# Performance work log

Hardware: AMD Instinct MI355X
Metric: run time of the kernel (lower is better)

## Reference

```python
import jax, jax.numpy as jnp
import numpy as np
import math

DIM = 2048
N_HEADS = 16
N_KV_HEADS = 8
HEAD_DIM = DIM // N_HEADS  # 128
N_REP = N_HEADS // N_KV_HEADS  # 2
BLOCK = 128
TOPK = 8
NEG_INF = -10000.0
SEQ = 4096
BS = 1


def _rope_tables(seq_len, head_dim, base=10000.0):
    inv_freq = 1.0 / (base ** (jnp.arange(0, head_dim, 2, dtype=jnp.float32) / head_dim))
    ang = jnp.arange(seq_len, dtype=jnp.float32)[:, None] * inv_freq[None, :]  # [S, hd/2]
    return jnp.cos(ang), jnp.sin(ang)


def _apply_rope(t, cos, sin):
    # t: [bs, S, h, hd]; interleaved pairs
    t1 = t[..., 0::2]
    t2 = t[..., 1::2]
    c = cos[None, :, None, :]
    s = sin[None, :, None, :]
    out_even = t1 * c - t2 * s
    out_odd = t1 * s + t2 * c
    out = jnp.stack([out_even, out_odd], axis=-1)  # [bs,S,h,hd/2,2]
    return out.reshape(t.shape)


def setup_inputs() -> dict:
    key = jax.random.key(0)
    ks = jax.random.split(key, 5)
    scale = 1.0 / math.sqrt(DIM)
    x = jax.random.normal(ks[0], (BS, SEQ, DIM), dtype=jnp.float32)
    wq = jax.random.normal(ks[1], (DIM, N_HEADS * HEAD_DIM), dtype=jnp.float32) * scale
    wk = jax.random.normal(ks[2], (DIM, N_KV_HEADS * HEAD_DIM), dtype=jnp.float32) * scale
    wv = jax.random.normal(ks[3], (DIM, N_KV_HEADS * HEAD_DIM), dtype=jnp.float32) * scale
    wo = jax.random.normal(ks[4], (DIM, DIM), dtype=jnp.float32) * scale
    return {"x": x, "wq": wq, "wk": wk, "wv": wv, "wo": wo}


def reference(x, wq, wk, wv, wo):
    bs, S, _ = x.shape
    inv_sqrt_d = 1.0 / math.sqrt(HEAD_DIM)

    q = (x @ wq).reshape(bs, S, N_HEADS, HEAD_DIM)
    k = (x @ wk).reshape(bs, S, N_KV_HEADS, HEAD_DIM)
    v = (x @ wv).reshape(bs, S, N_KV_HEADS, HEAD_DIM)

    cos, sin = _rope_tables(S, HEAD_DIM)
    q = _apply_rope(q, cos, sin)
    k = _apply_rope(k, cos, sin)

    # [bs, h, S, hd]
    q = jnp.transpose(q, (0, 2, 1, 3))
    k = jnp.transpose(k, (0, 2, 1, 3))
    v = jnp.transpose(v, (0, 2, 1, 3))

    # GQA expand (repeat_interleave over head dim)
    k_e = jnp.repeat(k, N_REP, axis=1)
    v_e = jnp.repeat(v, N_REP, axis=1)

    num_blocks = S // BLOCK  # 32, divides evenly (pad_len == 0)
    k_blocks = k_e.reshape(bs, N_HEADS, num_blocks, BLOCK, HEAD_DIM)
    block_means = k_blocks.mean(axis=3)  # [bs,h,nb,hd]

    gating = jnp.einsum('bhsd,bhnd->bhsn', q, block_means) * inv_sqrt_d
    q_block_idx = jnp.arange(S) // BLOCK
    future_block = q_block_idx[:, None] < jnp.arange(num_blocks)[None, :]  # [S, nb]
    gating = jnp.where(future_block[None, None], NEG_INF, gating)

    curr_k = min(TOPK, num_blocks)
    _, sel_idx = jax.lax.top_k(gating, curr_k)  # [bs,h,S,k]
    selected = jnp.sum(jax.nn.one_hot(sel_idx, num_blocks, dtype=jnp.float32), axis=-2) > 0  # [bs,h,S,nb]

    token_keep = jnp.repeat(selected, BLOCK, axis=-1)[..., :S]  # [bs,h,S,S]
    token_mask = jnp.where(token_keep, 0.0, NEG_INF)

    scores = jnp.einsum('bhsd,bhtd->bhst', q, k_e) * inv_sqrt_d
    causal = jnp.triu(jnp.ones((S, S), dtype=jnp.float32), k=1)  # 1 where future token
    # faithful to source: elementwise max of token mask and causal*neg_inf
    final_mask = jnp.maximum(token_mask, causal[None, None] * NEG_INF)
    scores = scores + final_mask

    probs = jax.nn.softmax(scores.astype(jnp.float32), axis=-1).astype(scores.dtype)
    out = jnp.einsum('bhst,bhtd->bhsd', probs, v_e)
    out = jnp.transpose(out, (0, 2, 1, 3)).reshape(bs, S, N_HEADS * HEAD_DIM)
    return out @ wo
```

## Files before the change

kernel.cpp:

```cpp
#include <hip/hip_runtime.h>
#include <hip/hip_fp16.h>

#define SQ   4096
#define DIMM 2048
#define QKVN 4096

typedef unsigned short u16;
typedef unsigned int u32;
typedef __attribute__((ext_vector_type(8))) short    short8;
typedef __attribute__((ext_vector_type(8))) _Float16 half8;
typedef __attribute__((ext_vector_type(4))) float    f32x4;

__device__ __forceinline__ u16 f2bf(float f) {
  u32 u = __float_as_uint(f);
  u32 r = u + 0x7fffu + ((u >> 16) & 1u);
  return (u16)(r >> 16);
}
__device__ __forceinline__ float bf2f(u16 h) { return __uint_as_float(((u32)h) << 16); }
__device__ __forceinline__ u16 f2h(float f) { return __half_as_ushort(__float2half(f)); }
__device__ __forceinline__ float h2f(u16 h) { union { u16 u; _Float16 f; } c; c.u = h; return (float)c.f; }

__device__ __forceinline__ void gll16(const void* g, void* l) {
  __builtin_amdgcn_global_load_lds((const __attribute__((address_space(1))) void*)g,
                                   (__attribute__((address_space(3))) void*)l, 16, 0, 0);
}

__device__ __host__ __forceinline__ int cidx(int qb) {
  return qb < 8 ? qb : qb < 16 ? 8 + (qb - 8) * 2 : qb < 24 ? 24 + (qb - 16) * 3 : 48 + (qb - 24) * 4;
}

__global__ __launch_bounds__(256) void k_tables(float* __restrict__ cosb, float* __restrict__ sinb) {
  int idx = blockIdx.x * 256 + threadIdx.x;
  int pos = idx >> 6, i = idx & 63;
  double f = 1.0 / pow(10000.0, (double)i / 64.0);
  float inv = (float)f;
  float ang = (float)pos * inv;
  cosb[idx] = (float)cos((double)ang);
  sinb[idx] = (float)sin((double)ang);
}

__global__ __launch_bounds__(256) void k_split_x(const float* __restrict__ x,
                                                 u16* __restrict__ xh, u16* __restrict__ xl) {
  size_t base = ((size_t)blockIdx.x * 256 + threadIdx.x) * 4;
  float4 v = *(const float4*)(x + base);
  float vv[4] = {v.x, v.y, v.z, v.w};
  u16 hh[4], ll[4];
#pragma unroll
  for (int j = 0; j < 4; j++) {
    hh[j] = f2bf(vv[j]);
    ll[j] = f2bf(vv[j] - bf2f(hh[j]));
  }
  *(uint2*)(xh + base) = make_uint2((u32)hh[0] | ((u32)hh[1] << 16), (u32)hh[2] | ((u32)hh[3] << 16));
  *(uint2*)(xl + base) = make_uint2((u32)ll[0] | ((u32)ll[1] << 16), (u32)ll[2] | ((u32)ll[3] << 16));
}

__global__ __launch_bounds__(256) void k_trans_split(const float* __restrict__ src, int N,
                                                     u16* __restrict__ dh, u16* __restrict__ dl,
                                                     int rowOff) {
  __shared__ float t[64][65];
  int n0 = blockIdx.x * 64, k0 = blockIdx.y * 64;
  int tid = threadIdx.x;
  int c = tid & 63, r4 = tid >> 6;
#pragma unroll
  for (int it = 0; it < 16; it++) {
    int kk = it * 4 + r4;
    t[kk][c] = src[(size_t)(k0 + kk) * N + n0 + c];
  }
  __syncthreads();
#pragma unroll
  for (int it = 0; it < 16; it++) {
    int nn = it * 4 + r4;
    float v = t[c][nn];
    u16 hh = f2bf(v);
    size_t o = (size_t)(rowOff + n0 + nn) * 2048 + k0 + c;
    dh[o] = hh;
    dl[o] = f2bf(v - bf2f(hh));
  }
}

__global__ __launch_bounds__(256) void k_trans_f16(const float* __restrict__ src, int N,
                                                   u16* __restrict__ dst) {
  __shared__ float t[64][65];
  int n0 = blockIdx.x * 64, k0 = blockIdx.y * 64;
  int tid = threadIdx.x;
  int c = tid & 63, r4 = tid >> 6;
#pragma unroll
  for (int it = 0; it < 16; it++) {
    int kk = it * 4 + r4;
    t[kk][c] = src[(size_t)(k0 + kk) * N + n0 + c];
  }
  __syncthreads();
#pragma unroll
  for (int it = 0; it < 16; it++) {
    int nn = it * 4 + r4;
    dst[(size_t)(n0 + nn) * 2048 + k0 + c] = f2h(t[c][nn]);
  }
}

__global__ __launch_bounds__(256) void k_gemm_qkv(
    const u16* __restrict__ xh, const u16* __restrict__ xl,
    const u16* __restrict__ wth, const u16* __restrict__ wtl,
    float* __restrict__ qkv) {
  __shared__ u16 lds[2][16384];
  const int tid = threadIdx.x;
  const int lane = tid & 63, wid = tid >> 6;
  const int rg = lane >> 4, c16 = lane & 15;
  const int bid0 = blockIdx.y * 32 + blockIdx.x;
  const int swz = (bid0 & 7) * 128 + (bid0 >> 3);
  const int m0 = (swz >> 5) * 128, n0 = (swz & 31) * 128;
  const int wm = wid >> 1, wn = wid & 1;
  const u16* gsrc = (wid == 0) ? xh + (size_t)m0 * 2048
                  : (wid == 1) ? xl + (size_t)m0 * 2048
                  : (wid == 2) ? wth + (size_t)n0 * 2048
                               : wtl + (size_t)n0 * 2048;
  const int srow4 = lane >> 2;
  const int pc = lane & 3;

  f32x4 acc[4][4];
#pragma unroll
  for (int a = 0; a < 4; a++)
#pragma unroll
    for (int b = 0; b < 4; b++) acc[a][b] = (f32x4){0.f, 0.f, 0.f, 0.f};

  auto stage = [&](int b, int k0) {
#pragma unroll
    for (int i = 0; i < 8; i++) {
      int r = i * 16 + srow4;
      int cl = pc ^ ((r >> 1) & 3);
      gll16(gsrc + (size_t)r * 2048 + k0 + cl * 8, &lds[b][wid * 4096 + i * 512 + lane * 8]);
    }
  };

  stage(0, 0);

  for (int ks = 0; ks < 64; ks++) {
    __syncthreads();
    if (ks + 1 < 64) stage((ks & 1) ^ 1, (ks + 1) * 32);
    const u16* lb = lds[ks & 1];

    short8 ah[4], al[4], bh[4], bl[4];
#pragma unroll
    for (int mf = 0; mf < 4; mf++) {
      int m = wm * 64 + mf * 16 + c16;
      int xo = m * 32 + ((rg ^ ((m >> 1) & 3)) * 8);
      ah[mf] = *(const short8*)(lb + xo);
      al[mf] = *(const short8*)(lb + 4096 + xo);
    }
#pragma unroll
    for (int nf = 0; nf < 4; nf++) {
      int n = wn * 64 + nf * 16 + c16;
      int xo = n * 32 + ((rg ^ ((n >> 1) & 3)) * 8);
      bh[nf] = *(const short8*)(lb + 8192 + xo);
      bl[nf] = *(const short8*)(lb + 12288 + xo);
    }
    __builtin_amdgcn_s_setprio(1);
#pragma unroll
    for (int mf = 0; mf < 4; mf++)
#pragma unroll
      for (int nf = 0; nf < 4; nf++) {
        acc[mf][nf] = __builtin_amdgcn_mfma_f32_16x16x32_bf16(ah[mf], bh[nf], acc[mf][nf], 0, 0, 0);
        acc[mf][nf] = __builtin_amdgcn_mfma_f32_16x16x32_bf16(ah[mf], bl[nf], acc[mf][nf], 0, 0, 0);
        acc[mf][nf] = __builtin_amdgcn_mfma_f32_16x16x32_bf16(al[mf], bh[nf], acc[mf][nf], 0, 0, 0);
      }
    __builtin_amdgcn_s_setprio(0);
  }
#pragma unroll
  for (int mf = 0; mf < 4; mf++)
#pragma unroll
    for (int nf = 0; nf < 4; nf++)
#pragma unroll
      for (int j = 0; j < 4; j++) {
        int m = m0 + wm * 64 + mf * 16 + rg * 4 + j;
        int n = n0 + wn * 64 + nf * 16 + c16;
        qkv[(size_t)m * QKVN + n] = acc[mf][nf][j];
      }
}

__global__ __launch_bounds__(256) void k_rope_qk(const float* __restrict__ qkv,
                                                 const float* __restrict__ cosb,
                                                 const float* __restrict__ sinb,
                                                 u16* __restrict__ qf, u16* __restrict__ kf2) {
  int idx = blockIdx.x * 256 + threadIdx.x;
  int i = idx & 63;
  int th = idx >> 6;
  int h = th % 24, t = th / 24;
  int c0 = (h < 16) ? h * 128 + 2 * i : 2048 + (h - 16) * 128 + 2 * i;
  float2 eo = *(const float2*)(qkv + (size_t)t * QKVN + c0);
  float c = cosb[t * 64 + i], s = sinb[t * 64 + i];
  float re = eo.x * c - eo.y * s;
  float ro = eo.x * s + eo.y * c;
  if (h < 16) {
    const float QSC = (float)(1.4426950408889634 * 0.08838834764831843);
    u32 pk = (u32)f2h(re * QSC) | ((u32)f2h(ro * QSC) << 16);
    *(u32*)(qf + ((size_t)h * SQ + t) * 128 + 2 * i) = pk;
  } else {
    int hk = h - 16;
    int d = 2 * i;
    int tile = t >> 6, tok = t & 63;
    int kk = tok >> 5, t5 = tok & 31;
    int hf = (t5 >> 2) & 1, c16v = ((t5 >> 3) << 2) | (t5 & 3);
    int dk = d >> 5, rg = (d >> 3) & 3, e = d & 7;
    int lane = rg * 16 + c16v, f = (kk * 2 + hf) * 4 + dk;
    u32 pk = (u32)f2h(re) | ((u32)f2h(ro) << 16);
    *(u32*)(kf2 + ((size_t)((hk * 64 + tile) * 16 + f) * 64 + lane) * 8 + e) = pk;
  }
}

__global__ __launch_bounds__(64) void k_bm(const float* __restrict__ qkv,
                                           const float* __restrict__ cosb,
                                           const float* __restrict__ sinb,
                                           float* __restrict__ bm) {
  int hk = blockIdx.x >> 5, n = blockIdx.x & 31;
  int i = threadIdx.x;
  double se = 0.0, so = 0.0;
  for (int t = 0; t < 128; t++) {
    int tt = n * 128 + t;
    float2 eo = *(const float2*)(qkv + (size_t)tt * QKVN + 2048 + hk * 128 + 2 * i);
    float c = cosb[tt * 64 + i], s = sinb[tt * 64 + i];
    se += (double)(eo.x * c - eo.y * s);
    so += (double)(eo.x * s + eo.y * c);
  }
  float* o = bm + ((size_t)(hk * 32 + n)) * 128 + 2 * i;
  o[0] = (float)(se * (1.0 / 128.0));
  o[1] = (float)(so * (1.0 / 128.0));
}

__global__ __launch_bounds__(64) void k_gate(const float* __restrict__ qkv,
                                             const float* __restrict__ cosb,
                                             const float* __restrict__ sinb,
                                             const float* __restrict__ bm,
                                             unsigned char* __restrict__ sel) {
  __shared__ float q[64][129];
  __shared__ float bml[32 * 128];
  int bz = blockIdx.x;
  int h = bz / 48;
  int rem = bz % 48;
  int b = 8 + (rem >> 1);
  int half = rem & 1;
  int tid = threadIdx.x;
  int hk = h >> 1;
  for (int rr = 0; rr < 64; rr++) {
    int ss = b * 128 + half * 64 + rr;
    float2 eo = *(const float2*)(qkv + (size_t)ss * QKVN + h * 128 + 2 * tid);
    float c = cosb[ss * 64 + tid], sn = sinb[ss * 64 + tid];
    q[rr][2 * tid]     = eo.x * c - eo.y * sn;
    q[rr][2 * tid + 1] = eo.x * sn + eo.y * c;
  }
  for (int o = tid; o < (b + 1) * 128; o += 64) bml[o] = bm[(size_t)hk * 32 * 128 + o];
  __syncthreads();
  int s = b * 128 + half * 64 + tid;
  double gb = 0.0;
  for (int d = 0; d < 128; d++) gb += (double)q[tid][d] * (double)bml[b * 128 + d];
  int cnt = 0;
  for (int n = 0; n < b; n++) {
    double g = 0.0;
    for (int d = 0; d < 128; d++) g += (double)q[tid][d] * (double)bml[n * 128 + d];
    cnt += (g >= gb) ? 1 : 0;
  }
  sel[h * SQ + s] = (cnt <= 7) ? 1 : 0;
}

__global__ __launch_bounds__(256) void k_vt2(const float* __restrict__ qkv, u16* __restrict__ vt2) {
  int hk = blockIdx.x & 7, tile = blockIdx.x >> 3;
  int tid = threadIdx.x;
  u16* dst = vt2 + (size_t)(hk * 64 + tile) * 8192;
#pragma unroll
  for (int rep = 0; rep < 16; rep++) {
    int idx = rep * 256 + tid;
    int tp = idx >> 7;
    int d  = idx & 127;
    int t  = tile * 64 + tp * 2;
    float v0 = qkv[(size_t)t * QKVN + 3072 + hk * 128 + d];
    float v1 = qkv[(size_t)(t + 1) * QKVN + 3072 + hk * 128 + d];
    int tok = tp * 2;
    int kk = tok >> 5, rg = (tok >> 3) & 3, e = tok & 7;
    int nf = d >> 4, c16v = d & 15;
    int lane = rg * 16 + c16v, g = kk * 8 + nf;
    u32 pk = (u32)f2h(v0) | ((u32)f2h(v1) << 16);
    *(u32*)(dst + ((size_t)(g * 64 + lane)) * 8 + e) = pk;
  }
}

__global__ __launch_bounds__(256) void k_attn_chunk(
    const u16* __restrict__ qf, const u16* __restrict__ kf2, const u16* __restrict__ vt2,
    const unsigned char* __restrict__ sel, u16* __restrict__ po, float* __restrict__ ml) {
  __shared__ u16 lds[2][8192];
  const int L = blockIdx.x;
  const int hk = L & 7;
  const int c = L >> 3;
  const int h = hk * 2 + (c & 1);
  const int cc = c >> 1;
  int qb, chunk;
  if (cc < 8)       { qb = cc;                   chunk = 0; }
  else if (cc < 24) { qb = 8 + ((cc - 8) >> 1);  chunk = (cc - 8) & 1; }
  else if (cc < 48) { qb = 16 + (cc - 24) / 3;   chunk = (cc - 24) % 3; }
  else              { qb = 24 + ((cc - 48) >> 2); chunk = (cc - 48) & 3; }
  const int nt128 = (qb < 8) ? 8 : (qb + 1);
  const int t0 = chunk * 32;
  const int t1 = (t0 + 32 < nt128 * 4) ? t0 + 32 : nt128 * 4;
  const int tid = threadIdx.x;
  const int lane = tid & 63, wid = tid >> 6;
  const int rg = lane >> 4, c16 = lane & 15;
  const bool hasMask = (qb >= 8);

  half8 aq[2][4];
#pragma unroll
  for (int mi = 0; mi < 2; mi++)
#pragma unroll
    for (int dk = 0; dk < 4; dk++) {
      int srow = qb * 128 + wid * 32 + mi * 16 + c16;
      aq[mi][dk] = *(const half8*)(qf + ((size_t)h * SQ + srow) * 128 + dk * 32 + rg * 8);
    }

  bool os2[2] = {true, true};
  if (hasMask) {
#pragma unroll
    for (int mi = 0; mi < 2; mi++)
      os2[mi] = sel[h * SQ + qb * 128 + wid * 32 + mi * 16 + c16] != 0;
  }

  f32x4 accO[2][8];
#pragma unroll
  for (int mi = 0; mi < 2; mi++)
#pragma unroll
    for (int nf = 0; nf < 8; nf++) accO[mi][nf] = (f32x4){0.f, 0.f, 0.f, 0.f};
  float mrun[2] = {-1e30f, -1e30f}, lrun[2] = {0.f, 0.f};

  const u16* kbase = kf2 + (size_t)hk * 64 * 8192;
  const u16* vbase = vt2 + (size_t)hk * 64 * 8192;

  auto stage = [&](int b, int n) {
    const u16* ks = kbase + (size_t)n * 4096;
    const u16* vs = vbase + (size_t)n * 4096;
#pragma unroll
    for (int r = 0; r < 2; r++) {
      gll16(ks + r * 2048 + wid * 512 + lane * 8, &lds[b][r * 2048 + wid * 512]);
      gll16(vs + r * 2048 + wid * 512 + lane * 8, &lds[b][4096 + r * 2048 + wid * 512]);
    }
  };

  stage(0, t0);

  for (int n = t0; n < t1; n++) {
    const int cur = (n - t0) & 1;
    __syncthreads();
    if (n + 1 < t1) stage(cur ^ 1, n + 1);
    const u16* lb = &lds[cur][0];

    f32x4 st[2][2];
#pragma unroll
    for (int hf = 0; hf < 2; hf++)
#pragma unroll
      for (int mi = 0; mi < 2; mi++) st[hf][mi] = (f32x4){0.f, 0.f, 0.f, 0.f};

    __builtin_amdgcn_s_setprio(1);
#pragma unroll
    for (int hf = 0; hf < 2; hf++) {
      half8 ka[4];
#pragma unroll
      for (int dk = 0; dk < 4; dk++)
        ka[dk] = *(const half8*)(lb + (hf * 4 + dk) * 512 + lane * 8);
#pragma unroll
      for (int dk = 0; dk < 4; dk++) {
        st[hf][0] = __builtin_amdgcn_mfma_f32_16x16x32_f16(ka[dk], aq[0][dk], st[hf][0], 0, 0, 0);
        st[hf][1] = __builtin_amdgcn_mfma_f32_16x16x32_f16(ka[dk], aq[1][dk], st[hf][1], 0, 0, 0);
      }
    }
    __builtin_amdgcn_s_setprio(0);

    if (hasMask && n >= 4 * qb) {
#pragma unroll
      for (int mi = 0; mi < 2; mi++) {
        if (!os2[mi]) {
          int row = qb * 128 + wid * 32 + mi * 16 + c16;
#pragma unroll
          for (int hf = 0; hf < 2; hf++)
#pragma unroll
            for (int j = 0; j < 4; j++) {
              int tg = n * 32 + rg * 8 + hf * 4 + j;
              if (tg > row) st[hf][mi][j] = -1e30f;
            }
        }
      }
    }

#pragma unroll
    for (int mi = 0; mi < 2; mi++) {
      float mt = st[0][mi][0];
#pragma unroll
      for (int hf = 0; hf < 2; hf++)
#pragma unroll
        for (int j = 0; j < 4; j++)
          if (hf | j) mt = fmaxf(mt, st[hf][mi][j]);
      mt = fmaxf(mt, __shfl_xor(mt, 16, 64));
      mt = fmaxf(mt, __shfl_xor(mt, 32, 64));
      if (!__all(mt <= mrun[mi] + 8.f)) {
        float mnew = fmaxf(mrun[mi], mt);
        float sc = exp2f(mrun[mi] - mnew);
        mrun[mi] = mnew;
        lrun[mi] *= sc;
#pragma unroll
        for (int nf = 0; nf < 8; nf++) accO[mi][nf] *= sc;
      }
      float ps = 0.f;
#pragma unroll
      for (int hf = 0; hf < 2; hf++)
#pragma unroll
        for (int j = 0; j < 4; j++) {
          float p = exp2f(st[hf][mi][j] - mrun[mi]);
          st[hf][mi][j] = p;
          ps += p;
        }
      ps += __shfl_xor(ps, 16, 64);
      ps += __shfl_xor(ps, 32, 64);
      lrun[mi] += ps;
    }

    half8 pa[2];
#pragma unroll
    for (int mi = 0; mi < 2; mi++) {
      union { half8 v; _Float16 e[8]; } pu;
#pragma unroll
      for (int hf = 0; hf < 2; hf++)
#pragma unroll
        for (int j = 0; j < 4; j++)
          pu.e[hf * 4 + j] = (_Float16)st[hf][mi][j];
      pa[mi] = pu.v;
    }

    __builtin_amdgcn_s_setprio(1);
#pragma unroll
    for (int nf = 0; nf < 8; nf++) {
      half8 va = *(const half8*)(lb + 4096 + nf * 512 + lane * 8);
      accO[0][nf] = __builtin_amdgcn_mfma_f32_16x16x32_f16(va, pa[0], accO[0][nf], 0, 0, 0);
      accO[1][nf] = __builtin_amdgcn_mfma_f32_16x16x32_f16(va, pa[1], accO[1][nf], 0, 0, 0);
    }
    __builtin_amdgcn_s_setprio(0);
  }

  const int pidx = h * 80 + cidx(qb) + chunk;
  u16* pob = po + (size_t)pidx * 16384;
#pragma unroll
  for (int mi = 0; mi < 2; mi++) {
    float inv = 1.0f / lrun[mi];
    int row = wid * 32 + mi * 16 + c16;
#pragma unroll
    for (int nf = 0; nf < 8; nf++) {
      u32 p0 = (u32)f2h(accO[mi][nf][0] * inv) | ((u32)f2h(accO[mi][nf][1] * inv) << 16);
      u32 p1 = (u32)f2h(accO[mi][nf][2] * inv) | ((u32)f2h(accO[mi][nf][3] * inv) << 16);
      *(uint2*)&pob[row * 128 + nf * 16 + rg * 4] = make_uint2(p0, p1);
    }
    if (rg == 0)
      ml[(size_t)pidx * 128 + row] = mrun[mi] + log2f(lrun[mi]);
  }
}

__global__ __launch_bounds__(256) void k_attn_combine(
    const u16* __restrict__ po, const float* __restrict__ ml, u16* __restrict__ attn) {
  const int qb = blockIdx.x, h = blockIdx.y;
  const int nc = (qb < 8) ? 1 : (qb < 16) ? 2 : (qb < 24) ? 3 : 4;
  const int base = h * 80 + cidx(qb);
  const int tid = threadIdx.x;
  const int r = tid >> 1, h64 = (tid & 1) * 64;
  float mp[4], M = -1e30f;
#pragma unroll
  for (int ci = 0; ci < 4; ci++) {
    mp[ci] = (ci < nc) ? ml[(size_t)(base + ci) * 128 + r] : -1e30f;
    M = fmaxf(M, mp[ci]);
  }
  float w[4], Ws = 0.f;
#pragma unroll
  for (int ci = 0; ci < 4; ci++) { w[ci] = exp2f(mp[ci] - M); Ws += (ci < nc) ? w[ci] : 0.f; }
  float inv = 1.0f / Ws;
  for (int d = 0; d < 64; d += 4) {
    float a[4] = {0.f, 0.f, 0.f, 0.f};
#pragma unroll
    for (int ci = 0; ci < 4; ci++) {
      if (ci < nc) {
        uint2 u = *(const uint2*)&po[(size_t)(base + ci) * 16384 + r * 128 + h64 + d];
        a[0] += w[ci] * h2f((u16)(u.x & 0xffff));
        a[1] += w[ci] * h2f((u16)(u.x >> 16));
        a[2] += w[ci] * h2f((u16)(u.y & 0xffff));
        a[3] += w[ci] * h2f((u16)(u.y >> 16));
      }
    }
    u32 p0 = (u32)f2h(a[0] * inv) | ((u32)f2h(a[1] * inv) << 16);
    u32 p1 = (u32)f2h(a[2] * inv) | ((u32)f2h(a[3] * inv) << 16);
    *(uint2*)&attn[(size_t)(qb * 128 + r) * DIMM + h * 128 + h64 + d] = make_uint2(p0, p1);
  }
}

__global__ __launch_bounds__(256) void k_gemm_out(
    const u16* __restrict__ attn, const u16* __restrict__ wot, float* __restrict__ out) {
  __shared__ u16 lds[2][8192];
  const int tid = threadIdx.x;
  const int lane = tid & 63, wid = tid >> 6;
  const int rg = lane >> 4, c16 = lane & 15;
  const int bid0 = blockIdx.y * 16 + blockIdx.x;
  const int swz = (bid0 & 7) * 64 + (bid0 >> 3);
  const int m0 = (swz >> 4) * 128, n0 = (swz & 15) * 128;
  const int wm = wid >> 1, wn = wid & 1;
  const u16* gsrc = (wid < 2) ? attn + (size_t)m0 * 2048 : wot + (size_t)n0 * 2048;
  const int obase = (wid < 2) ? 0 : 4096;
  const int i2base = (wid & 1) * 4;
  const int srow4 = lane >> 2;
  const int pc = lane & 3;

  f32x4 acc[4][4];
#pragma unroll
  for (int a = 0; a < 4; a++)
#pragma unroll
    for (int b = 0; b < 4; b++) acc[a][b] = (f32x4){0.f, 0.f, 0.f, 0.f};

  auto stage = [&](int b, int k0) {
#pragma unroll
    for (int i = 0; i < 4; i++) {
      int i2 = i2base + i;
      int r = i2 * 16 + srow4;
      int cl = pc ^ ((r >> 1) & 3);
      gll16(gsrc + (size_t)r * 2048 + k0 + cl * 8, &lds[b][obase + i2 * 512 + lane * 8]);
    }
  };

  stage(0, 0);

  for (int ks = 0; ks < 64; ks++) {
    __syncthreads();
    if (ks + 1 < 64) stage((ks & 1) ^ 1, (ks + 1) * 32);
    const u16* lb = lds[ks & 1];

    half8 a[4], b[4];
#pragma unroll
    for (int mf = 0; mf < 4; mf++) {
      int m = wm * 64 + mf * 16 + c16;
      a[mf] = *(const half8*)(lb + m * 32 + ((rg ^ ((m >> 1) & 3)) * 8));
    }
#pragma unroll
    for (int nf = 0; nf < 4; nf++) {
      int n = wn * 64 + nf * 16 + c16;
      b[nf] = *(const half8*)(lb + 4096 + n * 32 + ((rg ^ ((n >> 1) & 3)) * 8));
    }
    __builtin_amdgcn_s_setprio(1);
#pragma unroll
    for (int mf = 0; mf < 4; mf++)
#pragma unroll
      for (int nf = 0; nf < 4; nf++)
        acc[mf][nf] = __builtin_amdgcn_mfma_f32_16x16x32_f16(a[mf], b[nf], acc[mf][nf], 0, 0, 0);
    __builtin_amdgcn_s_setprio(0);
  }
#pragma unroll
  for (int mf = 0; mf < 4; mf++)
#pragma unroll
    for (int nf = 0; nf < 4; nf++)
#pragma unroll
      for (int j = 0; j < 4; j++) {
        int m = m0 + wm * 64 + mf * 16 + rg * 4 + j;
        int n = n0 + wn * 64 + nf * 16 + c16;
        out[(size_t)m * DIMM + n] = acc[mf][nf][j];
      }
}

extern "C" void kernel_launch(void* const* d_in, const int* in_sizes, int n_in,
                              void* d_out, int out_size, void* d_ws, size_t ws_size,
                              hipStream_t stream) {
  (void)in_sizes; (void)n_in; (void)out_size; (void)ws_size;
  const float* x  = (const float*)d_in[0];
  const float* wq = (const float*)d_in[1];
  const float* wk = (const float*)d_in[2];
  const float* wv = (const float*)d_in[3];
  const float* wo = (const float*)d_in[4];
  float* out = (float*)d_out;

  char* ws = (char*)d_ws;
  const size_t MB = 1024 * 1024;
  char* A = ws;
  u16*   xh  = (u16*)(A);
  u16*   xl  = (u16*)(A + 16 * MB);
  u16*   wth = (u16*)(A + 32 * MB);
  u16*   wtl = (u16*)(A + 48 * MB);
  float* qkv = (float*)(A + 64 * MB);
  u16*   po  = (u16*)(A);
  float* ml  = (float*)(A + 48 * MB);
  char* B = ws + 128 * MB;
  size_t off = 0;
  auto alloc = [&](size_t b) { char* p = B + off; off += (b + 255) & ~(size_t)255; return p; };
  u16*   wot  = (u16*)alloc((size_t)DIMM * DIMM * 2);
  float* cosb = (float*)alloc((size_t)SQ * 64 * 4);
  float* sinb = (float*)alloc((size_t)SQ * 64 * 4);
  u16*   qf   = (u16*)alloc((size_t)16 * SQ * 128 * 2);
  u16*   kf2  = (u16*)alloc((size_t)8 * SQ * 128 * 2);
  u16*   vt2  = (u16*)alloc((size_t)8 * 128 * SQ * 2);
  float* bm   = (float*)alloc((size_t)8 * 32 * 128 * 4);
  unsigned char* sel = (unsigned char*)alloc((size_t)16 * SQ);
  u16*   attn = (u16*)alloc((size_t)SQ * DIMM * 2);

  k_tables<<<SQ * 64 / 256, 256, 0, stream>>>(cosb, sinb);
  k_split_x<<<(SQ * DIMM) / (256 * 4), 256, 0, stream>>>(x, xh, xl);
  k_trans_split<<<dim3(32, 32), 256, 0, stream>>>(wq, 2048, wth, wtl, 0);
  k_trans_split<<<dim3(16, 32), 256, 0, stream>>>(wk, 1024, wth, wtl, 2048);
  k_trans_split<<<dim3(16, 32), 256, 0, stream>>>(wv, 1024, wth, wtl, 3072);
  k_trans_f16<<<dim3(32, 32), 256, 0, stream>>>(wo, 2048, wot);
  k_gemm_qkv<<<dim3(32, 32), 256, 0, stream>>>(xh, xl, wth, wtl, qkv);
  k_rope_qk<<<(SQ * 24 * 64) / 256, 256, 0, stream>>>(qkv, cosb, sinb, qf, kf2);
  k_vt2<<<512, 256, 0, stream>>>(qkv, vt2);
  k_bm<<<256, 64, 0, stream>>>(qkv, cosb, sinb, bm);
  k_gate<<<16 * 48, 64, 0, stream>>>(qkv, cosb, sinb, bm, sel);
  k_attn_chunk<<<1280, 256, 0, stream>>>(qf, kf2, vt2, sel, po, ml);
  k_attn_combine<<<dim3(32, 16), 256, 0, stream>>>(po, ml, attn);
  k_gemm_out<<<dim3(16, 32), 256, 0, stream>>>(attn, wot, out);
}
```

Measured before the change: 594.1 us.

## Load attention K/V fragments directly from global; single-buffer out-proj GEMM with K=64

The attention chunk kernel no longer stages K and V tiles through LDS with double buffering. Each wave now loads its MFMA fragments straight from global memory, which removes the LDS traffic and the per-iteration barrier but depends on the cache to serve reuse across the four waves. The output projection GEMM switches from a double-buffered K=32 pipeline to a single-buffered K=64 step with an 8-way XOR swizzle and two barriers per step. That halves the loop trip count but loses the overlap of the next tile's load with compute.

```diff
diff --git a/kernel.cpp b/kernel.cpp
--- a/kernel.cpp
+++ b/kernel.cpp
@@ -284,7 +284,6 @@
 __global__ __launch_bounds__(256) void k_attn_chunk(
     const u16* __restrict__ qf, const u16* __restrict__ kf2, const u16* __restrict__ vt2,
     const unsigned char* __restrict__ sel, u16* __restrict__ po, float* __restrict__ ml) {
-  __shared__ u16 lds[2][8192];
   const int L = blockIdx.x;
   const int hk = L & 7;
   const int c = L >> 3;
@@ -329,23 +328,9 @@
   const u16* kbase = kf2 + (size_t)hk * 64 * 8192;
   const u16* vbase = vt2 + (size_t)hk * 64 * 8192;
 
-  auto stage = [&](int b, int n) {
-    const u16* ks = kbase + (size_t)n * 4096;
-    const u16* vs = vbase + (size_t)n * 4096;
-#pragma unroll
-    for (int r = 0; r < 2; r++) {
-      gll16(ks + r * 2048 + wid * 512 + lane * 8, &lds[b][r * 2048 + wid * 512]);
-      gll16(vs + r * 2048 + wid * 512 + lane * 8, &lds[b][4096 + r * 2048 + wid * 512]);
-    }
-  };
-
-  stage(0, t0);
-
   for (int n = t0; n < t1; n++) {
-    const int cur = (n - t0) & 1;
-    __syncthreads();
-    if (n + 1 < t1) stage(cur ^ 1, n + 1);
-    const u16* lb = &lds[cur][0];
+    const u16* kt = kbase + (size_t)n * 4096;
+    const u16* vt = vbase + (size_t)n * 4096;
 
     f32x4 st[2][2];
 #pragma unroll
@@ -353,20 +338,27 @@
 #pragma unroll
       for (int mi = 0; mi < 2; mi++) st[hf][mi] = (f32x4){0.f, 0.f, 0.f, 0.f};
 
+    half8 ka[2][4];
+#pragma unroll
+    for (int hf = 0; hf < 2; hf++)
+#pragma unroll
+      for (int dk = 0; dk < 4; dk++)
+        ka[hf][dk] = *(const half8*)(kt + (hf * 4 + dk) * 512 + lane * 8);
+
     __builtin_amdgcn_s_setprio(1);
 #pragma unroll
-    for (int hf = 0; hf < 2; hf++) {
-      half8 ka[4];
-#pragma unroll
-      for (int dk = 0; dk < 4; dk++)
-        ka[dk] = *(const half8*)(lb + (hf * 4 + dk) * 512 + lane * 8);
+    for (int hf = 0; hf < 2; hf++)
 #pragma unroll
       for (int dk = 0; dk < 4; dk++) {
-        st[hf][0] = __builtin_amdgcn_mfma_f32_16x16x32_f16(ka[dk], aq[0][dk], st[hf][0], 0, 0, 0);
-        st[hf][1] = __builtin_amdgcn_mfma_f32_16x16x32_f16(ka[dk], aq[1][dk], st[hf][1], 0, 0, 0);
-      }
-    }
+        st[hf][0] = __builtin_amdgcn_mfma_f32_16x16x32_f16(ka[hf][dk], aq[0][dk], st[hf][0], 0, 0, 0);
+        st[hf][1] = __builtin_amdgcn_mfma_f32_16x16x32_f16(ka[hf][dk], aq[1][dk], st[hf][1], 0, 0, 0);
+      }
     __builtin_amdgcn_s_setprio(0);
+
+    half8 va[8];
+#pragma unroll
+    for (int nf = 0; nf < 8; nf++)
+      va[nf] = *(const half8*)(vt + nf * 512 + lane * 8);
 
     if (hasMask && n >= 4 * qb) {
 #pragma unroll
@@ -431,9 +423,8 @@
     __builtin_amdgcn_s_setprio(1);
 #pragma unroll
     for (int nf = 0; nf < 8; nf++) {
-      half8 va = *(const half8*)(lb + 4096 + nf * 512 + lane * 8);
-      accO[0][nf] = __builtin_amdgcn_mfma_f32_16x16x32_f16(va, pa[0], accO[0][nf], 0, 0, 0);
-      accO[1][nf] = __builtin_amdgcn_mfma_f32_16x16x32_f16(va, pa[1], accO[1][nf], 0, 0, 0);
+      accO[0][nf] = __builtin_amdgcn_mfma_f32_16x16x32_f16(va[nf], pa[0], accO[0][nf], 0, 0, 0);
+      accO[1][nf] = __builtin_amdgcn_mfma_f32_16x16x32_f16(va[nf], pa[1], accO[1][nf], 0, 0, 0);
     }
     __builtin_amdgcn_s_setprio(0);
   }
@@ -492,7 +483,7 @@
 
 __global__ __launch_bounds__(256) void k_gemm_out(
     const u16* __restrict__ attn, const u16* __restrict__ wot, float* __restrict__ out) {
-  __shared__ u16 lds[2][8192];
+  __shared__ u16 lds[2 * 128 * 64];
   const int tid = threadIdx.x;
   const int lane = tid & 63, wid = tid >> 6;
   const int rg = lane >> 4, c16 = lane & 15;
@@ -501,10 +492,7 @@
   const int m0 = (swz >> 4) * 128, n0 = (swz & 15) * 128;
   const int wm = wid >> 1, wn = wid & 1;
   const u16* gsrc = (wid < 2) ? attn + (size_t)m0 * 2048 : wot + (size_t)n0 * 2048;
-  const int obase = (wid < 2) ? 0 : 4096;
-  const int i2base = (wid & 1) * 4;
-  const int srow4 = lane >> 2;
-  const int pc = lane & 3;
+  const int sr = lane >> 3, scn = lane & 7;
 
   f32x4 acc[4][4];
 #pragma unroll
@@ -512,41 +500,37 @@
 #pragma unroll
     for (int b = 0; b < 4; b++) acc[a][b] = (f32x4){0.f, 0.f, 0.f, 0.f};
 
-  auto stage = [&](int b, int k0) {
-#pragma unroll
-    for (int i = 0; i < 4; i++) {
-      int i2 = i2base + i;
-      int r = i2 * 16 + srow4;
-      int cl = pc ^ ((r >> 1) & 3);
-      gll16(gsrc + (size_t)r * 2048 + k0 + cl * 8, &lds[b][obase + i2 * 512 + lane * 8]);
-    }
-  };
-
-  stage(0, 0);
-
-  for (int ks = 0; ks < 64; ks++) {
+  for (int k0 = 0; k0 < 2048; k0 += 64) {
+#pragma unroll
+    for (int i = 0; i < 8; i++) {
+      int slot = wid * 8 + i;
+      int s2 = slot & 15;
+      int r = s2 * 8 + sr;
+      int cs = (scn ^ (r & 7)) * 8;
+      gll16(gsrc + (size_t)r * 2048 + k0 + cs, lds + slot * 512);
+    }
     __syncthreads();
-    if (ks + 1 < 64) stage((ks & 1) ^ 1, (ks + 1) * 32);
-    const u16* lb = lds[ks & 1];
-
-    half8 a[4], b[4];
-#pragma unroll
-    for (int mf = 0; mf < 4; mf++) {
-      int m = wm * 64 + mf * 16 + c16;
-      a[mf] = *(const half8*)(lb + m * 32 + ((rg ^ ((m >> 1) & 3)) * 8));
-    }
-#pragma unroll
-    for (int nf = 0; nf < 4; nf++) {
-      int n = wn * 64 + nf * 16 + c16;
-      b[nf] = *(const half8*)(lb + 4096 + n * 32 + ((rg ^ ((n >> 1) & 3)) * 8));
-    }
-    __builtin_amdgcn_s_setprio(1);
-#pragma unroll
-    for (int mf = 0; mf < 4; mf++)
-#pragma unroll
-      for (int nf = 0; nf < 4; nf++)
-        acc[mf][nf] = __builtin_amdgcn_mfma_f32_16x16x32_f16(a[mf], b[nf], acc[mf][nf], 0, 0, 0);
-    __builtin_amdgcn_s_setprio(0);
+#pragma unroll
+    for (int kk = 0; kk < 2; kk++) {
+      half8 a[4], b[4];
+      int ch = kk * 4 + rg;
+#pragma unroll
+      for (int mf = 0; mf < 4; mf++) {
+        int m = wm * 64 + mf * 16 + c16;
+        a[mf] = *(const half8*)(lds + m * 64 + ((ch ^ (m & 7)) * 8));
+      }
+#pragma unroll
+      for (int nf = 0; nf < 4; nf++) {
+        int n = wn * 64 + nf * 16 + c16;
+        b[nf] = *(const half8*)(lds + 8192 + n * 64 + ((ch ^ (n & 7)) * 8));
+      }
+#pragma unroll
+      for (int mf = 0; mf < 4; mf++)
+#pragma unroll
+        for (int nf = 0; nf < 4; nf++)
+          acc[mf][nf] = __builtin_amdgcn_mfma_f32_16x16x32_f16(a[mf], b[nf], acc[mf][nf], 0, 0, 0);
+    }
+    __syncthreads();
   }
 #pragma unroll
   for (int mf = 0; mf < 4; mf++)
```

After: 572.0 us. -3.7%, faster.
